# Performance work log

Measured on AMD Instinct MI355X. Metric: run time of the kernel, lower is better.

## Reference

```python
import jax, jax.numpy as jnp
import numpy as np

S = 8192      # sequence length
E = 1024      # embeddingDimension
D = 64        # linearDimension


def setup_inputs() -> dict:
    key = jax.random.key(0)
    ks = jax.random.split(key, 9)
    lim = 1.0 / np.sqrt(E)
    inp = {
        "x": jax.random.normal(ks[0], (S, E), dtype=jnp.float32),
        "y": jax.random.normal(ks[1], (S, E), dtype=jnp.float32),
        "z": jax.random.normal(ks[2], (S, E), dtype=jnp.float32),
        "Wq": jax.random.uniform(ks[3], (E, D), jnp.float32, -lim, lim),
        "bq": jax.random.uniform(ks[4], (D,), jnp.float32, -lim, lim),
        "Wk": jax.random.uniform(ks[5], (E, D), jnp.float32, -lim, lim),
        "bk": jax.random.uniform(ks[6], (D,), jnp.float32, -lim, lim),
        "Wv": jax.random.uniform(ks[7], (E, D), jnp.float32, -lim, lim),
        "bv": jax.random.uniform(ks[8], (D,), jnp.float32, -lim, lim),
    }
    return inp


def reference(x, y, z, Wq, bq, Wk, bk, Wv, bv):
    q = x @ Wq + bq                      # [S, D]
    k = y @ Wk + bk                      # [S, D]
    v = z @ Wv + bv                      # [S, D]
    scores = q @ k.T                     # [S, S]
    n = scores.shape[0]
    # masked=True: add triu(-inf, diag=1) causal mask (faithful to torch.triu of a full -inf matrix)
    neg_inf = jnp.float32(-jnp.inf)
    causal = jnp.triu(jnp.full((n, n), neg_inf, dtype=scores.dtype), k=1)
    scores = scores + causal
    # original scales by sqrt(size(0)) = sqrt(seq_len), softmax over last dim (torch 2D default)
    attn = jax.nn.softmax(scores / jnp.sqrt(jnp.float32(n)), axis=-1)
    return attn @ v                      # [S, D]
```

## Files before the change

kernel.cpp:

```cpp
#include <hip/hip_runtime.h>

#define SEQ 8192
#define EMB 1024
#define DIM 64

typedef __attribute__((ext_vector_type(8))) short bf16x8;
typedef __attribute__((ext_vector_type(4))) float f32x4;
typedef __attribute__((ext_vector_type(16))) float f32x16;

#if __has_builtin(__builtin_amdgcn_exp2f)
#define EXP2 __builtin_amdgcn_exp2f
#else
#define EXP2 exp2f
#endif

#define SCL 0.0159396779f

__device__ inline unsigned short f2bf(float f) {
    union { float f; unsigned u; } x; x.f = f;
    unsigned r = x.u + 0x7FFFu + ((x.u >> 16) & 1u);
    return (unsigned short)(r >> 16);
}

__device__ inline unsigned cvtpk(float lo, float hi) {
    unsigned r;
    asm("v_cvt_pk_bf16_f32 %0, %1, %2" : "=v"(r) : "v"(lo), "v"(hi));
    return r;
}

__device__ __forceinline__ void gload16(const float* g, float* l) {
    __builtin_amdgcn_global_load_lds(
        (const __attribute__((address_space(1))) unsigned*)g,
        (__attribute__((address_space(3))) unsigned*)l, 16, 0, 0);
}


__global__ __launch_bounds__(256) void wt_kernel(
    const float* __restrict__ Wq, const float* __restrict__ Wk,
    const float* __restrict__ Wv, unsigned short* __restrict__ Wt)
{
    const int f = (int)blockIdx.x * 256 + (int)threadIdx.x;
    const int n    = f & 63;
    const int rest = f >> 6;
    const int mat  = rest >> 8;
    const int kp   = (rest & 255) * 4;
    const float* W = (mat == 0) ? Wq : (mat == 1) ? Wk : Wv;
    const int sg = kp >> 5, qq = (kp >> 3) & 3, j0 = kp & 7;
    const int wcg = n >> 4, c = n & 15;
    const int lanep = qq * 16 + c;
    float v0 = W[(size_t)(kp + 0) * DIM + n];
    float v1 = W[(size_t)(kp + 1) * DIM + n];
    float v2 = W[(size_t)(kp + 2) * DIM + n];
    float v3 = W[(size_t)(kp + 3) * DIM + n];
    uint2 pk;
    pk.x = cvtpk(v0, v1);
    pk.y = cvtpk(v2, v3);
    const size_t off = ((size_t)(((mat * 32 + sg) * 4 + wcg)) * 64 + lanep) * 8 + j0;
    *(uint2*)&Wt[off] = pk;
}

__device__ inline bf16x8 cvt8(float4 a, float4 b) {
    union { unsigned u[4]; bf16x8 v; } r;
    r.u[0] = cvtpk(a.x, a.y);
    r.u[1] = cvtpk(a.z, a.w);
    r.u[2] = cvtpk(b.x, b.y);
    r.u[3] = cvtpk(b.z, b.w);
    return r.v;
}

__global__ __launch_bounds__(512) void proj_kernel(
    const float* __restrict__ x, const float* __restrict__ y, const float* __restrict__ z,
    const float* __restrict__ bq, const float* __restrict__ bk, const float* __restrict__ bv,
    const unsigned short* __restrict__ Wt, unsigned short* __restrict__ qkv)
{
    __shared__ float tile[3][32][128];

    const int bid = (int)blockIdx.x;
    const int mat = bid >> 8;
    const int rb  = (bid & 255) * 32;

    const int tid  = (int)threadIdx.x;
    const int lane = tid & 63;
    const int w    = tid >> 6;
    const int wr   = w >> 2;
    const int wc   = w & 3;
    const int c    = lane & 15;
    const int qq   = lane >> 4;

    const float* X  = (mat == 0) ? x  : (mat == 1) ? y  : z;
    const float* Bv = (mat == 0) ? bq : (mat == 1) ? bk : bv;
    const unsigned short* Wm = Wt + (size_t)mat * 65536;
    unsigned short* outp = qkv + (size_t)mat * (SEQ * DIM);

    f32x4 acc = (f32x4){0.f, 0.f, 0.f, 0.f};

    const int arow = wr * 16 + c;
    const int swl  = arow & 7;
    const unsigned short* Wp = Wm + (size_t)wc * 512 + (size_t)lane * 8;
    const bool swapped = (mat == 1);

    const int sr0 = w * 4 + (lane >> 5);
    #define STAGE(nb, t)                                                        \
        {                                                                       \
            const int k0_ = (t) * 128;                                          \
            _Pragma("unroll")                                                   \
            for (int j = 0; j < 2; ++j) {                                       \
                const int r_ = sr0 + j * 2;                                     \
                const float* src_ = X + (size_t)(rb + r_) * EMB + k0_           \
                                      + (((lane & 31) ^ (r_ & 7)) << 2);        \
                gload16(src_, &tile[nb][w * 4 + j * 2][0]);                     \
            }                                                                   \
        }

    #define COMP(bt, t)                                                         \
        {                                                                       \
            const float* rowp = &tile[bt][arow][0];                             \
            _Pragma("unroll")                                                   \
            for (int s = 0; s < 4; ++s) {                                       \
                float4 fa = *(const float4*)(rowp + s * 32                      \
                                             + (((qq * 2)     ^ swl) << 2));    \
                float4 fb = *(const float4*)(rowp + s * 32                      \
                                             + (((qq * 2 + 1) ^ swl) << 2));    \
                bf16x8 af = cvt8(fa, fb);                                       \
                bf16x8 bfr = *(const bf16x8*)(Wp + (size_t)((t) * 4 + s) * 2048);\
                if (swapped)                                                    \
                    acc = __builtin_amdgcn_mfma_f32_16x16x32_bf16(bfr, af, acc, 0, 0, 0); \
                else                                                            \
                    acc = __builtin_amdgcn_mfma_f32_16x16x32_bf16(af, bfr, acc, 0, 0, 0); \
            }                                                                   \
        }

    STAGE(0, 0);
    STAGE(1, 1);
    STAGE(2, 2);

    #pragma unroll
    for (int t = 0; t < 8; ++t) {
        if (t <= 5)      asm volatile("s_waitcnt vmcnt(4)" ::: "memory");
        else if (t == 6) asm volatile("s_waitcnt vmcnt(2)" ::: "memory");
        else             asm volatile("s_waitcnt vmcnt(0)" ::: "memory");
        __builtin_amdgcn_s_barrier();
        COMP(t % 3, t);
        if (t < 5) {
            __builtin_amdgcn_s_barrier();
            STAGE(t % 3, t + 3);
        } else if (t < 7) {
            __builtin_amdgcn_s_barrier();
        }
    }
    #undef STAGE
    #undef COMP

    const int T = rb >> 5;
    if (mat == 0) {
        const int col = wc * 16 + c;
        const float bb = Bv[col];
        #pragma unroll
        for (int i = 0; i < 4; ++i) {
            const int row = rb + wr * 16 + qq * 4 + i;
            outp[(size_t)row * DIM + col] = f2bf(acc[i] + bb);
        }
    } else if (mat == 1) {
        f32x4 bb4 = *(const f32x4*)&Bv[wc * 16 + qq * 4];
        const int base = (((T * 4 + wc) * 2 + (qq >> 1)) * 32 + wr * 16 + c) * 8 + (qq & 1) * 4;
        uint2 pk;
        pk.x = cvtpk(acc[0] + bb4[0], acc[1] + bb4[1]);
        pk.y = cvtpk(acc[2] + bb4[2], acc[3] + bb4[3]);
        *(uint2*)&outp[base] = pk;
    } else {
        const float bb = Bv[wc * 16 + c];
        const int base = ((((T * 2 + wr) * 2 + (wc >> 1)) * 2 + (qq >> 1)) * 32
                          + (wc & 1) * 16 + c) * 8 + (qq & 1) * 4;
        uint2 pk;
        pk.x = cvtpk(acc[0] + bb, acc[1] + bb);
        pk.y = cvtpk(acc[2] + bb, acc[3] + bb);
        *(uint2*)&outp[base] = pk;
    }
}

__global__ __launch_bounds__(256, 3) void attn_kernel(
    const unsigned short* __restrict__ qkv, float* __restrict__ out,
    float* __restrict__ Opart, float* __restrict__ MLpart)
{
    const unsigned short* Q  = qkv;
    const unsigned short* KF = qkv + SEQ * DIM;
    const unsigned short* VF = qkv + 2 * SEQ * DIM;

    __shared__ float Oall[4][32][68];
    __shared__ float Ml[4][32][2];
    __shared__ float sScl[4][32];
    __shared__ float sM[32];
    __shared__ float sL[32];

    const int u = 1151 - (int)blockIdx.x;
    int g;
    if (u < 32) g = 0; else if (u < 96) g = 1; else if (u < 192) g = 2;
    else if (u < 320) g = 3; else if (u < 480) g = 4; else if (u < 672) g = 5;
    else if (u < 896) g = 6; else g = 7;
    const int o_  = u - 16 * g * (g + 1);
    const int qt  = 32 * g + o_ / (g + 1);
    const int cid = o_ - (o_ / (g + 1)) * (g + 1);

    const int m0 = qt * 32;
    const int tid = (int)threadIdx.x;
    const int lane = tid & 63;
    const int w = tid >> 6;
    const int col = lane & 31;
    const int hi = lane >> 5;

    bf16x8 qf[4];
    {
        const unsigned short* Qr = Q + (size_t)(m0 + col) * DIM + hi * 8;
        #pragma unroll
        for (int ks = 0; ks < 4; ++ks) qf[ks] = *(const bf16x8*)(Qr + ks * 16);
    }

    f32x16 o0, o1;
    #pragma unroll
    for (int r = 0; r < 16; ++r) { o0[r] = 0.f; o1[r] = 0.f; }
    float m_i = -1e30f, l_i = 0.f;

    const int nT = qt + 1;
    const int tb = cid * 32;
    const int te = (tb + 32 < nT) ? (tb + 32) : nT;
    const int nC = te - tb;
    const int w0 = tb + ((nC * w) >> 2);
    const int w1 = tb + ((nC * (w + 1)) >> 2);
    const int nW = w1 - w0;
    const int nP = nW >> 1;

    for (int pi = 0; pi < nP; ++pi) {
        const int t = w0 + 2 * pi;
        const unsigned short* kb = KF + (size_t)t * 2048 + (size_t)lane * 8;
        const unsigned short* vb_ = VF + (size_t)t * 2048 + (size_t)lane * 8;
        bf16x8 kA[4], kB[4];
        #pragma unroll
        for (int ks = 0; ks < 4; ++ks) kA[ks] = *(const bf16x8*)(kb + ks * 512);
        #pragma unroll
        for (int ks = 0; ks < 4; ++ks) kB[ks] = *(const bf16x8*)(kb + 2048 + ks * 512);
        bf16x8 va[4], vbf[4];
        #pragma unroll
        for (int i = 0; i < 4; ++i) va[i]  = *(const bf16x8*)(vb_ + i * 1024);
        #pragma unroll
        for (int i = 0; i < 4; ++i) vbf[i] = *(const bf16x8*)(vb_ + 512 + i * 1024);

        f32x16 sa, sb;
        #pragma unroll
        for (int r = 0; r < 16; ++r) { sa[r] = 0.f; sb[r] = 0.f; }
        __builtin_amdgcn_s_setprio(1);
        #pragma unroll
        for (int ks = 0; ks < 4; ++ks) {
            sa = __builtin_amdgcn_mfma_f32_32x32x16_bf16(kA[ks], qf[ks], sa, 0, 0, 0);
            sb = __builtin_amdgcn_mfma_f32_32x32x16_bf16(kB[ks], qf[ks], sb, 0, 0, 0);
        }
        __builtin_amdgcn_s_setprio(0);

        float p0[16], p1[16];
        #pragma unroll
        for (int r = 0; r < 16; ++r) { p0[r] = sa[r] * SCL; p1[r] = sb[r] * SCL; }
        if (t + 1 == qt) {
            #pragma unroll
            for (int r = 0; r < 16; ++r) {
                const int kvr = (r & 3) + 8 * (r >> 2) + 4 * hi;
                if (kvr > col) p1[r] = -1e30f;
            }
        }
        float tm = fmaxf(p0[0], p1[0]);
        #pragma unroll
        for (int r = 1; r < 16; ++r) tm = fmaxf(tm, fmaxf(p0[r], p1[r]));
        tm = fmaxf(tm, __shfl_xor(tm, 32));
        if (!__all(tm <= m_i + 2.0f)) {
            const float mn = fmaxf(m_i, tm);
            const float alpha = EXP2(m_i - mn);
            m_i = mn;
            l_i *= alpha;
            #pragma unroll
            for (int r = 0; r < 16; ++r) { o0[r] *= alpha; o1[r] *= alpha; }
        }
        float rs = 0.f;
        #pragma unroll
        for (int r = 0; r < 16; ++r) { p0[r] = EXP2(p0[r] - m_i); rs += p0[r]; }
        #pragma unroll
        for (int r = 0; r < 16; ++r) { p1[r] = EXP2(p1[r] - m_i); rs += p1[r]; }
        rs += __shfl_xor(rs, 32);
        l_i += rs;

        unsigned pwA[8], pwB[8];
        #pragma unroll
        for (int i = 0; i < 8; ++i) pwA[i] = cvtpk(p0[2 * i], p0[2 * i + 1]);
        #pragma unroll
        for (int i = 0; i < 8; ++i) pwB[i] = cvtpk(p1[2 * i], p1[2 * i + 1]);
        asm volatile("v_permlane32_swap_b32 %0, %1" : "+v"(pwA[0]), "+v"(pwA[2]));
        asm volatile("v_permlane32_swap_b32 %0, %1" : "+v"(pwA[1]), "+v"(pwA[3]));
        asm volatile("v_permlane32_swap_b32 %0, %1" : "+v"(pwA[4]), "+v"(pwA[6]));
        asm volatile("v_permlane32_swap_b32 %0, %1" : "+v"(pwA[5]), "+v"(pwA[7]));
        asm volatile("v_permlane32_swap_b32 %0, %1" : "+v"(pwB[0]), "+v"(pwB[2]));
        asm volatile("v_permlane32_swap_b32 %0, %1" : "+v"(pwB[1]), "+v"(pwB[3]));
        asm volatile("v_permlane32_swap_b32 %0, %1" : "+v"(pwB[4]), "+v"(pwB[6]));
        asm volatile("v_permlane32_swap_b32 %0, %1" : "+v"(pwB[5]), "+v"(pwB[7]));
        union { unsigned uu[4]; bf16x8 v; } pa0, pa1, pb0, pb1;
        pa0.uu[0] = pwA[0]; pa0.uu[1] = pwA[1]; pa0.uu[2] = pwA[2]; pa0.uu[3] = pwA[3];
        pa1.uu[0] = pwA[4]; pa1.uu[1] = pwA[5]; pa1.uu[2] = pwA[6]; pa1.uu[3] = pwA[7];
        pb0.uu[0] = pwB[0]; pb0.uu[1] = pwB[1]; pb0.uu[2] = pwB[2]; pb0.uu[3] = pwB[3];
        pb1.uu[0] = pwB[4]; pb1.uu[1] = pwB[5]; pb1.uu[2] = pwB[6]; pb1.uu[3] = pwB[7];

        __builtin_amdgcn_s_setprio(1);
        o0 = __builtin_amdgcn_mfma_f32_32x32x16_bf16(va[0],  pa0.v, o0, 0, 0, 0);
        o1 = __builtin_amdgcn_mfma_f32_32x32x16_bf16(vbf[0], pa0.v, o1, 0, 0, 0);
        o0 = __builtin_amdgcn_mfma_f32_32x32x16_bf16(va[1],  pa1.v, o0, 0, 0, 0);
        o1 = __builtin_amdgcn_mfma_f32_32x32x16_bf16(vbf[1], pa1.v, o1, 0, 0, 0);
        o0 = __builtin_amdgcn_mfma_f32_32x32x16_bf16(va[2],  pb0.v, o0, 0, 0, 0);
        o1 = __builtin_amdgcn_mfma_f32_32x32x16_bf16(vbf[2], pb0.v, o1, 0, 0, 0);
        o0 = __builtin_amdgcn_mfma_f32_32x32x16_bf16(va[3],  pb1.v, o0, 0, 0, 0);
        o1 = __builtin_amdgcn_mfma_f32_32x32x16_bf16(vbf[3], pb1.v, o1, 0, 0, 0);
        __builtin_amdgcn_s_setprio(0);
    }

    if (nW & 1) {
        const int t = w1 - 1;
        const unsigned short* kb = KF + (size_t)t * 2048 + (size_t)lane * 8;
        const unsigned short* vb_ = VF + (size_t)t * 2048 + (size_t)lane * 8;
        bf16x8 kA[4];
        #pragma unroll
        for (int ks = 0; ks < 4; ++ks) kA[ks] = *(const bf16x8*)(kb + ks * 512);
        bf16x8 va0 = *(const bf16x8*)(vb_);
        bf16x8 va1 = *(const bf16x8*)(vb_ + 1024);
        bf16x8 vb0 = *(const bf16x8*)(vb_ + 512);
        bf16x8 vb1 = *(const bf16x8*)(vb_ + 1536);

        f32x16 sa;
        #pragma unroll
        for (int r = 0; r < 16; ++r) sa[r] = 0.f;
        __builtin_amdgcn_s_setprio(1);
        #pragma unroll
        for (int ks = 0; ks < 4; ++ks)
            sa = __builtin_amdgcn_mfma_f32_32x32x16_bf16(kA[ks], qf[ks], sa, 0, 0, 0);
        __builtin_amdgcn_s_setprio(0);

        float p0[16];
        #pragma unroll
        for (int r = 0; r < 16; ++r) p0[r] = sa[r] * SCL;
        if (t == qt) {
            #pragma unroll
            for (int r = 0; r < 16; ++r) {
                const int kvr = (r & 3) + 8 * (r >> 2) + 4 * hi;
                if (kvr > col) p0[r] = -1e30f;
            }
        }
        float tm = p0[0];
        #pragma unroll
        for (int r = 1; r < 16; ++r) tm = fmaxf(tm, p0[r]);
        tm = fmaxf(tm, __shfl_xor(tm, 32));
        if (!__all(tm <= m_i + 2.0f)) {
            const float mn = fmaxf(m_i, tm);
            const float alpha = EXP2(m_i - mn);
            m_i = mn;
            l_i *= alpha;
            #pragma unroll
            for (int r = 0; r < 16; ++r) { o0[r] *= alpha; o1[r] *= alpha; }
        }
        float rs = 0.f;
        #pragma unroll
        for (int r = 0; r < 16; ++r) { p0[r] = EXP2(p0[r] - m_i); rs += p0[r]; }
        rs += __shfl_xor(rs, 32);
        l_i += rs;

        unsigned pwA[8];
        #pragma unroll
        for (int i = 0; i < 8; ++i) pwA[i] = cvtpk(p0[2 * i], p0[2 * i + 1]);
        asm volatile("v_permlane32_swap_b32 %0, %1" : "+v"(pwA[0]), "+v"(pwA[2]));
        asm volatile("v_permlane32_swap_b32 %0, %1" : "+v"(pwA[1]), "+v"(pwA[3]));
        asm volatile("v_permlane32_swap_b32 %0, %1" : "+v"(pwA[4]), "+v"(pwA[6]));
        asm volatile("v_permlane32_swap_b32 %0, %1" : "+v"(pwA[5]), "+v"(pwA[7]));
        union { unsigned uu[4]; bf16x8 v; } pa0, pa1;
        pa0.uu[0] = pwA[0]; pa0.uu[1] = pwA[1]; pa0.uu[2] = pwA[2]; pa0.uu[3] = pwA[3];
        pa1.uu[0] = pwA[4]; pa1.uu[1] = pwA[5]; pa1.uu[2] = pwA[6]; pa1.uu[3] = pwA[7];

        __builtin_amdgcn_s_setprio(1);
        o0 = __builtin_amdgcn_mfma_f32_32x32x16_bf16(va0, pa0.v, o0, 0, 0, 0);
        o1 = __builtin_amdgcn_mfma_f32_32x32x16_bf16(vb0, pa0.v, o1, 0, 0, 0);
        o0 = __builtin_amdgcn_mfma_f32_32x32x16_bf16(va1, pa1.v, o0, 0, 0, 0);
        o1 = __builtin_amdgcn_mfma_f32_32x32x16_bf16(vb1, pa1.v, o1, 0, 0, 0);
        __builtin_amdgcn_s_setprio(0);
    }

    #pragma unroll
    for (int r = 0; r < 16; ++r) {
        const int d = (r & 3) + 8 * (r >> 2) + 4 * hi;
        Oall[w][col][d]      = o0[r];
        Oall[w][col][32 + d] = o1[r];
    }
    if (hi == 0) { Ml[w][col][0] = m_i; Ml[w][col][1] = l_i; }
    __syncthreads();

    if (tid < 32) {
        float M = Ml[0][tid][0];
        #pragma unroll
        for (int w2 = 1; w2 < 4; ++w2) M = fmaxf(M, Ml[w2][tid][0]);
        sM[tid] = M;
    }
    __syncthreads();
    if (tid < 128) {
        const int w2 = tid >> 5, r = tid & 31;
        sScl[w2][r] = EXP2(Ml[w2][r][0] - sM[r]);
    }
    __syncthreads();
    if (tid < 32) {
        float L = 0.f;
        #pragma unroll
        for (int w2 = 0; w2 < 4; ++w2) L += Ml[w2][tid][1] * sScl[w2][tid];
        sL[tid] = L;
    }
    __syncthreads();

    const int r = tid >> 3;
    const int c0 = (tid & 7) * 8;
    f32x4 a0 = (f32x4){0.f, 0.f, 0.f, 0.f};
    f32x4 a1 = (f32x4){0.f, 0.f, 0.f, 0.f};
    #pragma unroll
    for (int w2 = 0; w2 < 4; ++w2) {
        const float sc = sScl[w2][r];
        const float* Orow = &Oall[w2][r][c0];
        a0 += (*(const f32x4*)(Orow)) * sc;
        a1 += (*(const f32x4*)(Orow + 4)) * sc;
    }
    if (qt < 32) {
        const float inv = 1.f / sL[r];
        float* op = out + (size_t)(m0 + r) * DIM + c0;
        *(f32x4*)(op)     = a0 * inv;
        *(f32x4*)(op + 4) = a1 * inv;
    } else {
        const int pb = 16 * (g - 1) * (g + 2) + (qt - 32 * g) * (g + 1) + cid;
        float* op = Opart + (size_t)pb * 2048 + r * 64 + c0;
        *(f32x4*)(op)     = a0;
        *(f32x4*)(op + 4) = a1;
        if (tid < 32) {
            MLpart[(size_t)pb * 64 + tid * 2]     = sM[tid];
            MLpart[(size_t)pb * 64 + tid * 2 + 1] = sL[tid];
        }
    }
}

__global__ __launch_bounds__(256) void fixup_kernel(
    const float* __restrict__ Opart, const float* __restrict__ MLpart,
    float* __restrict__ out)
{
    __shared__ float sScl[8][32];
    __shared__ float sInvL[32];

    const int qt = 32 + (int)blockIdx.x;
    const int g  = qt >> 5;
    const int nc = g + 1;
    const int pb = 16 * (g - 1) * (g + 2) + (qt - 32 * g) * nc;
    const int tid = (int)threadIdx.x;

    if (tid < 32) {
        float M = -1e30f;
        for (int c2 = 0; c2 < nc; ++c2)
            M = fmaxf(M, MLpart[(size_t)(pb + c2) * 64 + tid * 2]);
        float L = 0.f;
        for (int c2 = 0; c2 < nc; ++c2) {
            const float sc = EXP2(MLpart[(size_t)(pb + c2) * 64 + tid * 2] - M);
            sScl[c2][tid] = sc;
            L += MLpart[(size_t)(pb + c2) * 64 + tid * 2 + 1] * sc;
        }
        sInvL[tid] = 1.f / L;
    }
    __syncthreads();

    const int r = tid >> 3;
    const int c0 = (tid & 7) * 8;
    f32x4 a0 = (f32x4){0.f, 0.f, 0.f, 0.f};
    f32x4 a1 = (f32x4){0.f, 0.f, 0.f, 0.f};
    for (int c2 = 0; c2 < nc; ++c2) {
        const float sc = sScl[c2][r];
        const float* Op = Opart + (size_t)(pb + c2) * 2048 + r * 64 + c0;
        a0 += (*(const f32x4*)(Op)) * sc;
        a1 += (*(const f32x4*)(Op + 4)) * sc;
    }
    const float inv = sInvL[r];
    float* op = out + (size_t)(qt * 32 + r) * DIM + c0;
    *(f32x4*)(op)     = a0 * inv;
    *(f32x4*)(op + 4) = a1 * inv;
}

extern "C" void kernel_launch(void* const* d_in, const int* in_sizes, int n_in,
                              void* d_out, int out_size, void* d_ws, size_t ws_size,
                              hipStream_t stream) {
    const float* x  = (const float*)d_in[0];
    const float* y  = (const float*)d_in[1];
    const float* z  = (const float*)d_in[2];
    const float* Wq = (const float*)d_in[3];
    const float* bq = (const float*)d_in[4];
    const float* Wk = (const float*)d_in[5];
    const float* bk = (const float*)d_in[6];
    const float* Wv = (const float*)d_in[7];
    const float* bv = (const float*)d_in[8];

    unsigned short* qkv = (unsigned short*)d_ws;
    unsigned short* Wt  = (unsigned short*)((char*)d_ws + 3145728);
    float* Opart        = (float*)((char*)d_ws + 3538944);
    float* MLpart       = (float*)((char*)d_ws + 12713984);
    float* out          = (float*)d_out;

    hipLaunchKernelGGL(wt_kernel,    dim3(192),  dim3(256), 0, stream, Wq, Wk, Wv, Wt);
    hipLaunchKernelGGL(proj_kernel,  dim3(768),  dim3(512), 0, stream, x, y, z, bq, bk, bv, Wt, qkv);
    hipLaunchKernelGGL(attn_kernel,  dim3(1152), dim3(256), 0, stream, qkv, out, Opart, MLpart);
    hipLaunchKernelGGL(fixup_kernel, dim3(224),  dim3(256), 0, stream, Opart, MLpart, out);
}
```

Measured before the change: 59.99 us.

## Prefetch projection weights into registers and software-pipeline K loads in attention

In the QKV projection kernel, weight fragments are now double-buffered in registers and loaded one step ahead. The staging loop is restructured to issue the next tile load right after the barrier, which drops one barrier per iteration and moves from three tiles in flight to two. In the attention kernel, the K fragments for the next pair of tiles are prefetched while the current tile's softmax and PV work proceed, and V loads are moved after the QK MFMAs. The aim is to hide global-load latency behind compute, at the cost of more live registers and possibly lower occupancy.

```diff
diff --git a/kernel.cpp b/kernel.cpp
--- a/kernel.cpp
+++ b/kernel.cpp
@@ -99,6 +99,8 @@
     const unsigned short* Wp = Wm + (size_t)wc * 512 + (size_t)lane * 8;
     const bool swapped = (mat == 1);
 
+    bf16x8 wreg[2][4];
+
     const int sr0 = w * 4 + (lane >> 5);
     #define STAGE(nb, t)                                                        \
         {                                                                       \
@@ -112,6 +114,13 @@
             }                                                                   \
         }
 
+    #define WLOAD(slot, t)                                                      \
+        {                                                                       \
+            _Pragma("unroll")                                                   \
+            for (int s = 0; s < 4; ++s)                                         \
+                wreg[slot][s] = *(const bf16x8*)(Wp + (size_t)((t) * 4 + s) * 2048); \
+        }
+
     #define COMP(bt, t)                                                         \
         {                                                                       \
             const float* rowp = &tile[bt][arow][0];                             \
@@ -122,7 +131,7 @@
                 float4 fb = *(const float4*)(rowp + s * 32                      \
                                              + (((qq * 2 + 1) ^ swl) << 2));    \
                 bf16x8 af = cvt8(fa, fb);                                       \
-                bf16x8 bfr = *(const bf16x8*)(Wp + (size_t)((t) * 4 + s) * 2048);\
+                bf16x8 bfr = wreg[(t) & 1][s];                                  \
                 if (swapped)                                                    \
                     acc = __builtin_amdgcn_mfma_f32_16x16x32_bf16(bfr, af, acc, 0, 0, 0); \
                 else                                                            \
@@ -131,24 +140,22 @@
         }
 
     STAGE(0, 0);
+    WLOAD(0, 0);
+    asm volatile("" ::: "memory");
     STAGE(1, 1);
-    STAGE(2, 2);
+    WLOAD(1, 1);
 
     #pragma unroll
     for (int t = 0; t < 8; ++t) {
-        if (t <= 5)      asm volatile("s_waitcnt vmcnt(4)" ::: "memory");
-        else if (t == 6) asm volatile("s_waitcnt vmcnt(2)" ::: "memory");
-        else             asm volatile("s_waitcnt vmcnt(0)" ::: "memory");
+        if (t < 7) asm volatile("s_waitcnt vmcnt(6)" ::: "memory");
+        else       asm volatile("s_waitcnt vmcnt(0)" ::: "memory");
         __builtin_amdgcn_s_barrier();
+        if (t < 6) STAGE((t + 2) % 3, t + 2);
         COMP(t % 3, t);
-        if (t < 5) {
-            __builtin_amdgcn_s_barrier();
-            STAGE(t % 3, t + 3);
-        } else if (t < 7) {
-            __builtin_amdgcn_s_barrier();
-        }
+        if (t < 6) WLOAD(t & 1, t + 2);
     }
     #undef STAGE
+    #undef WLOAD
     #undef COMP
 
     const int T = rb >> 5;
@@ -229,20 +236,17 @@
     const int nW = w1 - w0;
     const int nP = nW >> 1;
 
+    bf16x8 kA[4], kB[4];
+    if (nP > 0) {
+        const unsigned short* kb0 = KF + (size_t)w0 * 2048 + (size_t)lane * 8;
+        #pragma unroll
+        for (int ks = 0; ks < 4; ++ks) kA[ks] = *(const bf16x8*)(kb0 + ks * 512);
+        #pragma unroll
+        for (int ks = 0; ks < 4; ++ks) kB[ks] = *(const bf16x8*)(kb0 + 2048 + ks * 512);
+    }
+
     for (int pi = 0; pi < nP; ++pi) {
         const int t = w0 + 2 * pi;
-        const unsigned short* kb = KF + (size_t)t * 2048 + (size_t)lane * 8;
-        const unsigned short* vb_ = VF + (size_t)t * 2048 + (size_t)lane * 8;
-        bf16x8 kA[4], kB[4];
-        #pragma unroll
-        for (int ks = 0; ks < 4; ++ks) kA[ks] = *(const bf16x8*)(kb + ks * 512);
-        #pragma unroll
-        for (int ks = 0; ks < 4; ++ks) kB[ks] = *(const bf16x8*)(kb + 2048 + ks * 512);
-        bf16x8 va[4], vbf[4];
-        #pragma unroll
-        for (int i = 0; i < 4; ++i) va[i]  = *(const bf16x8*)(vb_ + i * 1024);
-        #pragma unroll
-        for (int i = 0; i < 4; ++i) vbf[i] = *(const bf16x8*)(vb_ + 512 + i * 1024);
 
         f32x16 sa, sb;
         #pragma unroll
@@ -254,6 +258,21 @@
             sb = __builtin_amdgcn_mfma_f32_32x32x16_bf16(kB[ks], qf[ks], sb, 0, 0, 0);
         }
         __builtin_amdgcn_s_setprio(0);
+
+        if (pi + 1 < nP) {
+            const unsigned short* kbn = KF + (size_t)(t + 2) * 2048 + (size_t)lane * 8;
+            #pragma unroll
+            for (int ks = 0; ks < 4; ++ks) kA[ks] = *(const bf16x8*)(kbn + ks * 512);
+            #pragma unroll
+            for (int ks = 0; ks < 4; ++ks) kB[ks] = *(const bf16x8*)(kbn + 2048 + ks * 512);
+        }
+
+        const unsigned short* vb_ = VF + (size_t)t * 2048 + (size_t)lane * 8;
+        bf16x8 va[4], vbf[4];
+        #pragma unroll
+        for (int i = 0; i < 4; ++i) va[i]  = *(const bf16x8*)(vb_ + i * 1024);
+        #pragma unroll
+        for (int i = 0; i < 4; ++i) vbf[i] = *(const bf16x8*)(vb_ + 512 + i * 1024);
 
         float p0[16], p1[16];
         #pragma unroll
@@ -320,9 +339,9 @@
         const int t = w1 - 1;
         const unsigned short* kb = KF + (size_t)t * 2048 + (size_t)lane * 8;
         const unsigned short* vb_ = VF + (size_t)t * 2048 + (size_t)lane * 8;
-        bf16x8 kA[4];
-        #pragma unroll
-        for (int ks = 0; ks < 4; ++ks) kA[ks] = *(const bf16x8*)(kb + ks * 512);
+        bf16x8 kT[4];
+        #pragma unroll
+        for (int ks = 0; ks < 4; ++ks) kT[ks] = *(const bf16x8*)(kb + ks * 512);
         bf16x8 va0 = *(const bf16x8*)(vb_);
         bf16x8 va1 = *(const bf16x8*)(vb_ + 1024);
         bf16x8 vb0 = *(const bf16x8*)(vb_ + 512);
@@ -334,7 +353,7 @@
         __builtin_amdgcn_s_setprio(1);
         #pragma unroll
         for (int ks = 0; ks < 4; ++ks)
-            sa = __builtin_amdgcn_mfma_f32_32x32x16_bf16(kA[ks], qf[ks], sa, 0, 0, 0);
+            sa = __builtin_amdgcn_mfma_f32_32x32x16_bf16(kT[ks], qf[ks], sa, 0, 0, 0);
         __builtin_amdgcn_s_setprio(0);
 
         float p0[16];
```

After: 57.41 us. 1.04x faster.
